# Kernel tuning notes

Hardware: AMD Instinct MI355X
Metric: run time of the kernel (lower is better)

## Reference

```python
import jax, jax.numpy as jnp
import numpy as np

NUM_CODEBOOKS = 8
CODEBOOK_SIZE = 256
DIM = 128
COMMITMENT_WEIGHT = 0.25
B, T = 16, 16384


def setup_inputs() -> dict:
    key = jax.random.key(0)
    k_z, k_cb = jax.random.split(key)
    z = jax.random.normal(k_z, (B, T, DIM), dtype=jnp.float32)
    # nn.init.uniform_(emb.weight, -1/codebook_size, 1/codebook_size)
    bound = 1.0 / CODEBOOK_SIZE
    codebooks = jax.random.uniform(
        k_cb, (NUM_CODEBOOKS, CODEBOOK_SIZE, DIM), dtype=jnp.float32,
        minval=-bound, maxval=bound)
    return {"z": z, "codebooks": codebooks}


def reference(z, codebooks):
    """Residual vector quantization.

    z: [B, T, D] float32
    codebooks: [K, C, D] float32
    Returns (quantized [B,T,D], indices [B,T,K] int32, vq_loss scalar).
    """
    sg = jax.lax.stop_gradient
    residual = z
    vq_loss = jnp.zeros((), dtype=z.dtype)
    quant_sum = jnp.zeros_like(z)
    all_indices = []
    for k in range(NUM_CODEBOOKS):
        cb = codebooks[k]                                   # [C, D]
        # squared euclidean distances: ||r||^2 + ||e||^2 - 2 r.e
        x_sq = jnp.sum(residual * residual, axis=-1, keepdims=True)   # [B,T,1]
        e_sq = jnp.sum(cb * cb, axis=-1)                               # [C]
        cross = jnp.einsum('btd,cd->btc', residual, cb)                # [B,T,C]
        distances = x_sq + e_sq[None, None, :] - 2.0 * cross           # [B,T,C]
        indices = jnp.argmin(distances, axis=-1)                       # [B,T]
        all_indices.append(indices)
        z_q = cb[indices]                                              # [B,T,D] gather
        codebook_loss = jnp.mean((sg(z_q) - residual) ** 2)
        commit_loss = jnp.mean((z_q - sg(residual)) ** 2)
        vq_loss = vq_loss + codebook_loss + COMMITMENT_WEIGHT * commit_loss
        quant_sum = quant_sum + z_q
        residual = residual - sg(z_q)
    indices_stacked = jnp.stack(all_indices, axis=-1)                  # [B,T,K]
    # straight-through estimator
    quantized = z + sg(quant_sum - z)
    return quantized, indices_stacked, vq_loss
```

## Files before the change

### kernel.cpp

```cpp
#include <hip/hip_runtime.h>
#include <hip/hip_bf16.h>
#include <math.h>
#include <float.h>

#define NUM_CB 8
#define CB_SIZE 256
#define DIM 128
#define BT (16 * 16384)
#define Q_ELEMS ((size_t)BT * DIM)
#define I_ELEMS ((size_t)BT * NUM_CB)

#define TC 64
#define TILES_PER_CB (CB_SIZE / TC)
#define TILE_BYTES 32768

#define MARGIN_A 1.5e-4f

typedef short  bf16x8 __attribute__((ext_vector_type(8)));
typedef float  f32x4  __attribute__((ext_vector_type(4)));

__device__ __forceinline__ unsigned short bf16_rne(float f) {
    unsigned int u = __float_as_uint(f);
    u = u + 0x7FFFu + ((u >> 16) & 1u);
    return (unsigned short)(u >> 16);
}
__device__ __forceinline__ float bf16_tof(unsigned short h) {
    return __uint_as_float(((unsigned int)h) << 16);
}
__device__ __forceinline__ unsigned short f2bf(float f) {
    __hip_bfloat16 h = __float2bfloat16(f);
    return *reinterpret_cast<unsigned short*>(&h);
}

__device__ __forceinline__ float np_sum_sq_128(const float* a) {
#pragma clang fp contract(off)
    float r0 = 0.f, r1 = 0.f, r2 = 0.f, r3 = 0.f,
          r4 = 0.f, r5 = 0.f, r6 = 0.f, r7 = 0.f;
#pragma unroll
    for (int i = 0; i < DIM; i += 8) {
        r0 = r0 + a[i + 0] * a[i + 0];
        r1 = r1 + a[i + 1] * a[i + 1];
        r2 = r2 + a[i + 2] * a[i + 2];
        r3 = r3 + a[i + 3] * a[i + 3];
        r4 = r4 + a[i + 4] * a[i + 4];
        r5 = r5 + a[i + 5] * a[i + 5];
        r6 = r6 + a[i + 6] * a[i + 6];
        r7 = r7 + a[i + 7] * a[i + 7];
    }
    return ((r0 + r1) + (r2 + r3)) + ((r4 + r5) + (r6 + r7));
}

__global__ void rvq_esq_kernel(const float* __restrict__ cb,
                               float* __restrict__ esq) {
    int i = blockIdx.x * blockDim.x + threadIdx.x;
    if (i >= NUM_CB * CB_SIZE) return;
    esq[i] = np_sum_sq_128(cb + (size_t)i * DIM);
}

__global__ void rvq_transpose_kernel(const float* __restrict__ cb,
                                     float* __restrict__ cbT) {
    int idx = blockIdx.x * blockDim.x + threadIdx.x;
    if (idx >= NUM_CB * DIM * CB_SIZE) return;
    int c = idx & (CB_SIZE - 1);
    int d = (idx >> 8) & (DIM - 1);
    int k = idx >> 15;
    cbT[idx] = cb[((size_t)(k * CB_SIZE + c)) * DIM + d];
}

__global__ void rvq_split_kernel(const float* __restrict__ cb,
                                 bf16x8* __restrict__ g_img) {
    int idx = blockIdx.x * blockDim.x + threadIdx.x;
    if (idx >= NUM_CB * CB_SIZE * 16) return;
    int slot = idx & 15;
    int cand = (idx >> 4) & (TC - 1);
    int t    = idx >> 10;
    const float* src = cb + ((size_t)t * TC + cand) * DIM + slot * 8;
    float4 a = *reinterpret_cast<const float4*>(src);
    float4 b = *reinterpret_cast<const float4*>(src + 4);
    float e[8] = {a.x, a.y, a.z, a.w, b.x, b.y, b.z, b.w};
    bf16x8 eh, el;
#pragma unroll
    for (int i = 0; i < 8; ++i) {
        unsigned short h = bf16_rne(e[i]);
        float rem = e[i] - bf16_tof(h);
        eh[i] = (short)h;
        el[i] = (short)bf16_rne(rem);
    }
    int ds = slot ^ (cand & 15);
    g_img[(size_t)t * 2048 + cand * 16 + ds]        = eh;
    g_img[(size_t)t * 2048 + 1024 + cand * 16 + ds] = el;
}

__device__ __forceinline__ void stage_tile(const bf16x8* __restrict__ g_img,
                                           bf16x8 (*s_buf)[2048],
                                           int t, int nb, int wid, int lane) {
    const char* gt = (const char*)g_img + (size_t)t * TILE_BYTES
                     + wid * 4096 + lane * 16;
    const char* lb = (const char*)(&s_buf[nb][0]) + wid * 4096;
#pragma unroll
    for (int c = 0; c < 4; ++c) {
        __builtin_amdgcn_global_load_lds(
            (const __attribute__((address_space(1))) unsigned int*)(gt + c * 1024),
            (__attribute__((address_space(3))) unsigned int*)(lb + c * 1024),
            16, 0, 0);
    }
}

__global__ __launch_bounds__(512, 2) void rvq_mfma_kernel(
    const float* __restrict__ z,
    const float* __restrict__ cb,
    const float* __restrict__ cbT,
    const float* __restrict__ esq,
    const bf16x8* __restrict__ g_img,
    float* __restrict__ out_q,
    float* __restrict__ out_idx,
    double* __restrict__ loss_acc) {

    __shared__ bf16x8 s_buf[2][2048];
    __shared__ __align__(16) float s_rbuf[8][DIM];
    __shared__ double s_wsum[8];

    const int tid  = threadIdx.x;
    const int wid  = tid >> 6;
    const int lane = tid & 63;
    const int lrow = lane & 15;
    const int lq   = lane >> 4;
    const int tokw = blockIdx.x * 128 + wid * 16;
    const int tok  = tokw + lrow;

    float r[4][8];
    {
        const float* zp = z + (size_t)tok * DIM + 8 * lq;
#pragma unroll
        for (int s = 0; s < 4; ++s) {
            float4 a = *reinterpret_cast<const float4*>(zp + 32 * s);
            float4 b = *reinterpret_cast<const float4*>(zp + 32 * s + 4);
            r[s][0] = a.x; r[s][1] = a.y; r[s][2] = a.z; r[s][3] = a.w;
            r[s][4] = b.x; r[s][5] = b.y; r[s][6] = b.z; r[s][7] = b.w;
        }
    }

    bf16x8 ah[4], am[4];
#pragma unroll
    for (int s = 0; s < 4; ++s)
#pragma unroll
        for (int i = 0; i < 8; ++i) {
            unsigned short h = f2bf(r[s][i]);
            float rem = r[s][i] - bf16_tof(h);
            ah[s][i] = (short)h;
            am[s][i] = (short)f2bf(rem);
        }

    double lsum = 0.0;

    stage_tile(g_img, s_buf, 0, 0, wid, lane);
    asm volatile("s_waitcnt vmcnt(0)" ::: "memory");
    __syncthreads();

    for (int k = 0; k < NUM_CB; ++k) {
        const float* esqk = esq + k * CB_SIZE;
        const float* cbk  = cb  + (size_t)k * CB_SIZE * DIM;
        const float* cbTk = cbT + (size_t)k * DIM * CB_SIZE + lane;

        float m1 = FLT_MAX, m2 = FLT_MAX;
        int   i1 = 0x7fffffff;

#pragma unroll
        for (int T = 0; T < TILES_PER_CB; ++T) {
            const int t  = k * TILES_PER_CB + T;
            const int nb = T & 1;
            if (k < NUM_CB - 1 || T < TILES_PER_CB - 1)
                stage_tile(g_img, s_buf, t + 1, nb ^ 1, wid, lane);

#pragma unroll
            for (int ctl = 0; ctl < 4; ++ctl) {
                const int ctg  = T * 4 + ctl;
                const int base = (ctl * 16 + lrow) * 16;
                bf16x8 bh[4], bl[4];
#pragma unroll
                for (int s = 0; s < 4; ++s) {
                    int ls = (4 * s + lq) ^ lrow;
                    bh[s] = s_buf[nb][base + ls];
                    bl[s] = s_buf[nb][1024 + base + ls];
                }
                f32x4 acc0 = {0.f, 0.f, 0.f, 0.f};
                f32x4 acc1 = {0.f, 0.f, 0.f, 0.f};
                acc0 = __builtin_amdgcn_mfma_f32_16x16x32_bf16(bh[0], ah[0], acc0, 0, 0, 0);
                acc0 = __builtin_amdgcn_mfma_f32_16x16x32_bf16(bh[1], ah[1], acc0, 0, 0, 0);
                acc1 = __builtin_amdgcn_mfma_f32_16x16x32_bf16(bh[2], ah[2], acc1, 0, 0, 0);
                acc1 = __builtin_amdgcn_mfma_f32_16x16x32_bf16(bh[3], ah[3], acc1, 0, 0, 0);
                acc0 = __builtin_amdgcn_mfma_f32_16x16x32_bf16(bh[0], am[0], acc0, 0, 0, 0);
                acc0 = __builtin_amdgcn_mfma_f32_16x16x32_bf16(bh[1], am[1], acc0, 0, 0, 0);
                acc1 = __builtin_amdgcn_mfma_f32_16x16x32_bf16(bh[2], am[2], acc1, 0, 0, 0);
                acc1 = __builtin_amdgcn_mfma_f32_16x16x32_bf16(bh[3], am[3], acc1, 0, 0, 0);
                acc0 = __builtin_amdgcn_mfma_f32_16x16x32_bf16(bl[0], ah[0], acc0, 0, 0, 0);
                acc0 = __builtin_amdgcn_mfma_f32_16x16x32_bf16(bl[1], ah[1], acc0, 0, 0, 0);
                acc1 = __builtin_amdgcn_mfma_f32_16x16x32_bf16(bl[2], ah[2], acc1, 0, 0, 0);
                acc1 = __builtin_amdgcn_mfma_f32_16x16x32_bf16(bl[3], ah[3], acc1, 0, 0, 0);

                float4 ev = *reinterpret_cast<const float4*>(
                    esqk + ctg * 16 + 4 * lq);
                const float es[4] = {ev.x, ev.y, ev.z, ev.w};
                const int cb0 = ctg * 16 + 4 * lq;
#pragma unroll
                for (int j = 0; j < 4; ++j) {
                    float s = fmaf(-2.0f, acc0[j] + acc1[j], es[j]);
                    m2 = fminf(m2, fmaxf(m1, s));
                    if (s < m1) { m1 = s; i1 = cb0 + j; }
                }
            }

            if (T == TILES_PER_CB - 1) {
#pragma unroll
                for (int d = 16; d < 64; d <<= 1) {
                    float om1 = __shfl_xor(m1, d);
                    float om2 = __shfl_xor(m2, d);
                    int   oi1 = __shfl_xor(i1, d);
                    bool ow = (om1 < m1) || (om1 == m1 && oi1 < i1);
                    float lo = ow ? m1 : om1;
                    m1 = ow ? om1 : m1;
                    i1 = ow ? oi1 : i1;
                    m2 = fminf(fminf(m2, om2), lo);
                }
                int cmin = i1;

                bool amb = !(m2 - m1 > MARGIN_A);
                unsigned long long mask = __ballot(amb && lane < 16);
                while (mask) {
                    int srct = __ffsll(mask) - 1;
                    mask &= mask - 1;
                    if (lrow == srct) {
#pragma unroll
                        for (int s = 0; s < 4; ++s) {
                            float4* dst = reinterpret_cast<float4*>(
                                &s_rbuf[wid][32 * s + 8 * lq]);
                            dst[0] = make_float4(r[s][0], r[s][1], r[s][2], r[s][3]);
                            dst[1] = make_float4(r[s][4], r[s][5], r[s][6], r[s][7]);
                        }
                    }
                    asm volatile("s_waitcnt lgkmcnt(0)" ::: "memory");
                    float xs = 0.f;
                    if (lane == 0) xs = np_sum_sq_128(&s_rbuf[wid][0]);
                    xs = __shfl(xs, 0);

                    const float* rb = &s_rbuf[wid][0];
                    float a0 = 0.f, a1 = 0.f, a2 = 0.f, a3 = 0.f;
#pragma unroll 8
                    for (int d = 0; d < DIM; ++d) {
                        float rv = rb[d];
                        const float* row = cbTk + (size_t)d * CB_SIZE;
                        a0 = fmaf(rv, row[0],   a0);
                        a1 = fmaf(rv, row[64],  a1);
                        a2 = fmaf(rv, row[128], a2);
                        a3 = fmaf(rv, row[192], a3);
                    }
                    float dd0, dd1, dd2, dd3;
                    {
#pragma clang fp contract(off)
                        float S0 = xs + esqk[lane];
                        float S1 = xs + esqk[lane + 64];
                        float S2 = xs + esqk[lane + 128];
                        float S3 = xs + esqk[lane + 192];
                        dd0 = S0 - 2.0f * a0;
                        dd1 = S1 - 2.0f * a1;
                        dd2 = S2 - 2.0f * a2;
                        dd3 = S3 - 2.0f * a3;
                    }
                    float bd = dd0; int bc = lane;
                    if (dd1 < bd) { bd = dd1; bc = lane + 64; }
                    if (dd2 < bd) { bd = dd2; bc = lane + 128; }
                    if (dd3 < bd) { bd = dd3; bc = lane + 192; }
#pragma unroll
                    for (int d = 1; d < 64; d <<= 1) {
                        float od = __shfl_xor(bd, d);
                        int   oc = __shfl_xor(bc, d);
                        if (od < bd || (od == bd && oc < bc)) { bd = od; bc = oc; }
                    }
                    if (lrow == srct) cmin = bc;
                }

                if (lane < 16)
                    out_idx[(size_t)(tokw + lane) * NUM_CB + k] = (float)cmin;

                const float* ep = cbk + (size_t)cmin * DIM + 8 * lq;
                float l0 = 0.f, l1 = 0.f, l2 = 0.f, l3 = 0.f;
#pragma unroll
                for (int s = 0; s < 4; ++s) {
                    float4 ev0 = *reinterpret_cast<const float4*>(ep + 32 * s);
                    float4 ev1 = *reinterpret_cast<const float4*>(ep + 32 * s + 4);
                    float d0 = ev0.x - r[s][0], d1 = ev0.y - r[s][1];
                    float d2 = ev0.z - r[s][2], d3 = ev0.w - r[s][3];
                    float d4 = ev1.x - r[s][4], d5 = ev1.y - r[s][5];
                    float d6 = ev1.z - r[s][6], d7 = ev1.w - r[s][7];
                    l0 = fmaf(d0, d0, l0); l1 = fmaf(d1, d1, l1);
                    l2 = fmaf(d2, d2, l2); l3 = fmaf(d3, d3, l3);
                    l0 = fmaf(d4, d4, l0); l1 = fmaf(d5, d5, l1);
                    l2 = fmaf(d6, d6, l2); l3 = fmaf(d7, d7, l3);
                    r[s][0] -= ev0.x; r[s][1] -= ev0.y; r[s][2] -= ev0.z; r[s][3] -= ev0.w;
                    r[s][4] -= ev1.x; r[s][5] -= ev1.y; r[s][6] -= ev1.z; r[s][7] -= ev1.w;
                }
                lsum += (double)((l0 + l1) + (l2 + l3));

                if (k < NUM_CB - 1) {
#pragma unroll
                    for (int s = 0; s < 4; ++s)
#pragma unroll
                        for (int i = 0; i < 8; ++i) {
                            unsigned short h = f2bf(r[s][i]);
                            float rem = r[s][i] - bf16_tof(h);
                            ah[s][i] = (short)h;
                            am[s][i] = (short)f2bf(rem);
                        }
                }
            }

            asm volatile("s_waitcnt vmcnt(0)" ::: "memory");
            __syncthreads();
        }
    }

    {
        const float* zp = z + (size_t)tok * DIM + 8 * lq;
        float* op = out_q + (size_t)tok * DIM + 8 * lq;
#pragma unroll
        for (int s = 0; s < 4; ++s) {
            float4 a = *reinterpret_cast<const float4*>(zp + 32 * s);
            float4 b = *reinterpret_cast<const float4*>(zp + 32 * s + 4);
            *reinterpret_cast<float4*>(op + 32 * s) =
                make_float4(a.x - r[s][0], a.y - r[s][1],
                            a.z - r[s][2], a.w - r[s][3]);
            *reinterpret_cast<float4*>(op + 32 * s + 4) =
                make_float4(b.x - r[s][4], b.y - r[s][5],
                            b.z - r[s][6], b.w - r[s][7]);
        }
    }

    for (int off = 32; off > 0; off >>= 1)
        lsum += __shfl_down(lsum, off, 64);
    if (lane == 0) s_wsum[wid] = lsum;
    __syncthreads();
    if (tid == 0) {
        double t = 0.0;
#pragma unroll
        for (int w = 0; w < 8; ++w) t += s_wsum[w];
        atomicAdd(loss_acc, t);
    }
}

__global__ void rvq_finalize_kernel(const double* __restrict__ loss_acc,
                                    float* __restrict__ out_loss) {
    out_loss[0] = (float)(1.25 * loss_acc[0] / (double)Q_ELEMS);
}

extern "C" void kernel_launch(void* const* d_in, const int* in_sizes, int n_in,
                              void* d_out, int out_size, void* d_ws, size_t ws_size,
                              hipStream_t stream) {
    const float* z  = (const float*)d_in[0];
    const float* cb = (const float*)d_in[1];

    float* out_q    = (float*)d_out;
    float* out_idx  = out_q + Q_ELEMS;
    float* out_loss = out_idx + I_ELEMS;

    double* loss_acc = (double*)d_ws;
    float*  esq      = (float*)((char*)d_ws + 256);
    bf16x8* g_img    = (bf16x8*)((char*)d_ws + 65536);
    float*  cbT      = (float*)((char*)d_ws + 65536 + 1048576);

    hipMemsetAsync(loss_acc, 0, sizeof(double), stream);
    rvq_esq_kernel<<<(NUM_CB * CB_SIZE + 255) / 256, 256, 0, stream>>>(cb, esq);
    rvq_split_kernel<<<(NUM_CB * CB_SIZE * 16 + 255) / 256, 256, 0, stream>>>(
        cb, g_img);
    rvq_transpose_kernel<<<(NUM_CB * DIM * CB_SIZE + 255) / 256, 256, 0,
                           stream>>>(cb, cbT);
    rvq_mfma_kernel<<<BT / 128, 512, 0, stream>>>(z, cb, cbT, esq, g_img,
                                                  out_q, out_idx, loss_acc);
    rvq_finalize_kernel<<<1, 1, 0, stream>>>(loss_acc, out_loss);
}
```

Measured before the change: 918.2 us.

## Switch distance GEMM to 32x32x16 MFMA with 32 tokens per wave

Measured after the change: 1.018 ms. 10.8% more time.

```diff
diff --git a/kernel.cpp b/kernel.cpp
--- a/kernel.cpp
+++ b/kernel.cpp
@@ -17,7 +17,7 @@
 #define MARGIN_A 1.5e-4f
 
 typedef short  bf16x8 __attribute__((ext_vector_type(8)));
-typedef float  f32x4  __attribute__((ext_vector_type(4)));
+typedef float  f32x16 __attribute__((ext_vector_type(16)));
 
 __device__ __forceinline__ unsigned short bf16_rne(float f) {
     unsigned int u = __float_as_uint(f);
@@ -55,6 +55,18 @@
     int i = blockIdx.x * blockDim.x + threadIdx.x;
     if (i >= NUM_CB * CB_SIZE) return;
     esq[i] = np_sum_sq_128(cb + (size_t)i * DIM);
+}
+
+__global__ void rvq_esqpk_kernel(const float* __restrict__ esq,
+                                 float* __restrict__ esq_pk) {
+    int idx = blockIdx.x * blockDim.x + threadIdx.x;
+    if (idx >= NUM_CB * 8 * 64 * 16) return;
+    int reg  = idx & 15;
+    int lane = (idx >> 4) & 63;
+    int til  = (idx >> 10) & 7;
+    int k    = idx >> 13;
+    esq_pk[idx] = esq[k * CB_SIZE + til * 32 +
+                      (reg & 3) + 8 * (reg >> 2) + 4 * (lane >> 5)];
 }
 
 __global__ void rvq_transpose_kernel(const float* __restrict__ cb,
@@ -95,10 +107,10 @@
                                            bf16x8 (*s_buf)[2048],
                                            int t, int nb, int wid, int lane) {
     const char* gt = (const char*)g_img + (size_t)t * TILE_BYTES
-                     + wid * 4096 + lane * 16;
-    const char* lb = (const char*)(&s_buf[nb][0]) + wid * 4096;
-#pragma unroll
-    for (int c = 0; c < 4; ++c) {
+                     + wid * 8192 + lane * 16;
+    const char* lb = (const char*)(&s_buf[nb][0]) + wid * 8192;
+#pragma unroll
+    for (int c = 0; c < 8; ++c) {
         __builtin_amdgcn_global_load_lds(
             (const __attribute__((address_space(1))) unsigned int*)(gt + c * 1024),
             (__attribute__((address_space(3))) unsigned int*)(lb + c * 1024),
@@ -106,49 +118,49 @@
     }
 }
 
-__global__ __launch_bounds__(512, 2) void rvq_mfma_kernel(
+__global__ __launch_bounds__(256) void rvq_mfma_kernel(
     const float* __restrict__ z,
     const float* __restrict__ cb,
     const float* __restrict__ cbT,
     const float* __restrict__ esq,
+    const float* __restrict__ esq_pk,
     const bf16x8* __restrict__ g_img,
     float* __restrict__ out_q,
     float* __restrict__ out_idx,
     double* __restrict__ loss_acc) {
 
     __shared__ bf16x8 s_buf[2][2048];
-    __shared__ __align__(16) float s_rbuf[8][DIM];
-    __shared__ double s_wsum[8];
+    __shared__ __align__(16) float s_rbuf[4][DIM];
+    __shared__ double s_wsum[4];
 
     const int tid  = threadIdx.x;
     const int wid  = tid >> 6;
     const int lane = tid & 63;
-    const int lrow = lane & 15;
-    const int lq   = lane >> 4;
-    const int tokw = blockIdx.x * 128 + wid * 16;
-    const int tok  = tokw + lrow;
-
-    float r[4][8];
+    const int tk   = lane & 31;
+    const int half = lane >> 5;
+    const int tokw = blockIdx.x * 128 + wid * 32;
+    const int tok  = tokw + tk;
+
+    float r[8][8];
     {
-        const float* zp = z + (size_t)tok * DIM + 8 * lq;
-#pragma unroll
-        for (int s = 0; s < 4; ++s) {
-            float4 a = *reinterpret_cast<const float4*>(zp + 32 * s);
-            float4 b = *reinterpret_cast<const float4*>(zp + 32 * s + 4);
+        const float* zp = z + (size_t)tok * DIM + 8 * half;
+#pragma unroll
+        for (int s = 0; s < 8; ++s) {
+            float4 a = *reinterpret_cast<const float4*>(zp + 16 * s);
+            float4 b = *reinterpret_cast<const float4*>(zp + 16 * s + 4);
             r[s][0] = a.x; r[s][1] = a.y; r[s][2] = a.z; r[s][3] = a.w;
             r[s][4] = b.x; r[s][5] = b.y; r[s][6] = b.z; r[s][7] = b.w;
         }
     }
 
-    bf16x8 ah[4], am[4];
-#pragma unroll
-    for (int s = 0; s < 4; ++s)
+    bf16x8 rh[8], rm[8];
+#pragma unroll
+    for (int s = 0; s < 8; ++s)
 #pragma unroll
         for (int i = 0; i < 8; ++i) {
             unsigned short h = f2bf(r[s][i]);
-            float rem = r[s][i] - bf16_tof(h);
-            ah[s][i] = (short)h;
-            am[s][i] = (short)f2bf(rem);
+            rh[s][i] = (short)h;
+            rm[s][i] = (short)f2bf(r[s][i] - bf16_tof(h));
         }
 
     double lsum = 0.0;
@@ -173,69 +185,68 @@
                 stage_tile(g_img, s_buf, t + 1, nb ^ 1, wid, lane);
 
 #pragma unroll
-            for (int ctl = 0; ctl < 4; ++ctl) {
-                const int ctg  = T * 4 + ctl;
-                const int base = (ctl * 16 + lrow) * 16;
-                bf16x8 bh[4], bl[4];
-#pragma unroll
-                for (int s = 0; s < 4; ++s) {
-                    int ls = (4 * s + lq) ^ lrow;
-                    bh[s] = s_buf[nb][base + ls];
-                    bl[s] = s_buf[nb][1024 + base + ls];
-                }
-                f32x4 acc0 = {0.f, 0.f, 0.f, 0.f};
-                f32x4 acc1 = {0.f, 0.f, 0.f, 0.f};
-                acc0 = __builtin_amdgcn_mfma_f32_16x16x32_bf16(bh[0], ah[0], acc0, 0, 0, 0);
-                acc0 = __builtin_amdgcn_mfma_f32_16x16x32_bf16(bh[1], ah[1], acc0, 0, 0, 0);
-                acc1 = __builtin_amdgcn_mfma_f32_16x16x32_bf16(bh[2], ah[2], acc1, 0, 0, 0);
-                acc1 = __builtin_amdgcn_mfma_f32_16x16x32_bf16(bh[3], ah[3], acc1, 0, 0, 0);
-                acc0 = __builtin_amdgcn_mfma_f32_16x16x32_bf16(bh[0], am[0], acc0, 0, 0, 0);
-                acc0 = __builtin_amdgcn_mfma_f32_16x16x32_bf16(bh[1], am[1], acc0, 0, 0, 0);
-                acc1 = __builtin_amdgcn_mfma_f32_16x16x32_bf16(bh[2], am[2], acc1, 0, 0, 0);
-                acc1 = __builtin_amdgcn_mfma_f32_16x16x32_bf16(bh[3], am[3], acc1, 0, 0, 0);
-                acc0 = __builtin_amdgcn_mfma_f32_16x16x32_bf16(bl[0], ah[0], acc0, 0, 0, 0);
-                acc0 = __builtin_amdgcn_mfma_f32_16x16x32_bf16(bl[1], ah[1], acc0, 0, 0, 0);
-                acc1 = __builtin_amdgcn_mfma_f32_16x16x32_bf16(bl[2], ah[2], acc1, 0, 0, 0);
-                acc1 = __builtin_amdgcn_mfma_f32_16x16x32_bf16(bl[3], ah[3], acc1, 0, 0, 0);
-
-                float4 ev = *reinterpret_cast<const float4*>(
-                    esqk + ctg * 16 + 4 * lq);
-                const float es[4] = {ev.x, ev.y, ev.z, ev.w};
-                const int cb0 = ctg * 16 + 4 * lq;
-#pragma unroll
-                for (int j = 0; j < 4; ++j) {
-                    float s = fmaf(-2.0f, acc0[j] + acc1[j], es[j]);
-                    m2 = fminf(m2, fmaxf(m1, s));
-                    if (s < m1) { m1 = s; i1 = cb0 + j; }
+            for (int u = 0; u < 2; ++u) {
+                const int til = T * 2 + u;
+                const int cand_img = u * 32 + tk;
+                float eq[16];
+                {
+                    const float4* ep4 = reinterpret_cast<const float4*>(
+                        esq_pk + (((size_t)(k * 8 + til) * 64 + lane) * 16));
+#pragma unroll
+                    for (int j = 0; j < 4; ++j) {
+                        float4 v = ep4[j];
+                        eq[4 * j + 0] = v.x; eq[4 * j + 1] = v.y;
+                        eq[4 * j + 2] = v.z; eq[4 * j + 3] = v.w;
+                    }
+                }
+                f32x16 acca = {0.f, 0.f, 0.f, 0.f, 0.f, 0.f, 0.f, 0.f,
+                               0.f, 0.f, 0.f, 0.f, 0.f, 0.f, 0.f, 0.f};
+                f32x16 accb = acca;
+#pragma unroll
+                for (int s = 0; s < 8; ++s) {
+                    const int ls = (2 * s + half) ^ (tk & 15);
+                    bf16x8 eh = s_buf[nb][cand_img * 16 + ls];
+                    bf16x8 el = s_buf[nb][1024 + cand_img * 16 + ls];
+                    acca = __builtin_amdgcn_mfma_f32_32x32x16_bf16(eh, rh[s], acca, 0, 0, 0);
+                    accb = __builtin_amdgcn_mfma_f32_32x32x16_bf16(eh, rm[s], accb, 0, 0, 0);
+                    accb = __builtin_amdgcn_mfma_f32_32x32x16_bf16(el, rh[s], accb, 0, 0, 0);
+                }
+#pragma unroll
+                for (int reg = 0; reg < 16; ++reg) {
+                    const int c = til * 32 + (reg & 3) + 8 * (reg >> 2) + 4 * half;
+                    float sc = fmaf(-2.0f, acca[reg] + accb[reg], eq[reg]);
+                    m2 = __builtin_amdgcn_fmed3f(m1, m2, sc);
+                    if (sc < m1) { i1 = c; }
+                    m1 = fminf(m1, sc);
                 }
             }
 
             if (T == TILES_PER_CB - 1) {
-#pragma unroll
-                for (int d = 16; d < 64; d <<= 1) {
-                    float om1 = __shfl_xor(m1, d);
-                    float om2 = __shfl_xor(m2, d);
-                    int   oi1 = __shfl_xor(i1, d);
-                    bool ow = (om1 < m1) || (om1 == m1 && oi1 < i1);
-                    float lo = ow ? m1 : om1;
-                    m1 = ow ? om1 : m1;
-                    i1 = ow ? oi1 : i1;
-                    m2 = fminf(fminf(m2, om2), lo);
+                {
+                    float o1 = __shfl_xor(m1, 32);
+                    float o2 = __shfl_xor(m2, 32);
+                    int   oi = __shfl_xor(i1, 32);
+                    bool ow = (o1 < m1) || (o1 == m1 && oi < i1);
+                    float lo = ow ? m1 : o1;
+                    m1 = ow ? o1 : m1;
+                    i1 = ow ? oi : i1;
+                    m2 = fminf(fminf(m2, o2), lo);
                 }
                 int cmin = i1;
 
                 bool amb = !(m2 - m1 > MARGIN_A);
-                unsigned long long mask = __ballot(amb && lane < 16);
+                unsigned long long mask = __ballot(amb && lane < 32);
                 while (mask) {
                     int srct = __ffsll(mask) - 1;
                     mask &= mask - 1;
-                    if (lrow == srct) {
-#pragma unroll
-                        for (int s = 0; s < 4; ++s) {
-                            float4* dst = reinterpret_cast<float4*>(
-                                &s_rbuf[wid][32 * s + 8 * lq]);
-                            dst[0] = make_float4(r[s][0], r[s][1], r[s][2], r[s][3]);
-                            dst[1] = make_float4(r[s][4], r[s][5], r[s][6], r[s][7]);
+                    if (tk == srct) {
+#pragma unroll
+                        for (int s = 0; s < 8; ++s) {
+                            float* dst = &s_rbuf[wid][16 * s + 8 * half];
+                            *reinterpret_cast<float4*>(dst) =
+                                make_float4(r[s][0], r[s][1], r[s][2], r[s][3]);
+                            *reinterpret_cast<float4*>(dst + 4) =
+                                make_float4(r[s][4], r[s][5], r[s][6], r[s][7]);
                         }
                     }
                     asm volatile("s_waitcnt lgkmcnt(0)" ::: "memory");
@@ -276,18 +287,18 @@
                         int   oc = __shfl_xor(bc, d);
                         if (od < bd || (od == bd && oc < bc)) { bd = od; bc = oc; }
                     }
-                    if (lrow == srct) cmin = bc;
-                }
-
-                if (lane < 16)
+                    if (tk == srct) cmin = bc;
+                }
+
+                if (lane < 32)
                     out_idx[(size_t)(tokw + lane) * NUM_CB + k] = (float)cmin;
 
-                const float* ep = cbk + (size_t)cmin * DIM + 8 * lq;
+                const float* ep = cbk + (size_t)cmin * DIM + 8 * half;
                 float l0 = 0.f, l1 = 0.f, l2 = 0.f, l3 = 0.f;
 #pragma unroll
-                for (int s = 0; s < 4; ++s) {
-                    float4 ev0 = *reinterpret_cast<const float4*>(ep + 32 * s);
-                    float4 ev1 = *reinterpret_cast<const float4*>(ep + 32 * s + 4);
+                for (int s = 0; s < 8; ++s) {
+                    float4 ev0 = *reinterpret_cast<const float4*>(ep + 16 * s);
+                    float4 ev1 = *reinterpret_cast<const float4*>(ep + 16 * s + 4);
                     float d0 = ev0.x - r[s][0], d1 = ev0.y - r[s][1];
                     float d2 = ev0.z - r[s][2], d3 = ev0.w - r[s][3];
                     float d4 = ev1.x - r[s][4], d5 = ev1.y - r[s][5];
@@ -303,13 +314,12 @@
 
                 if (k < NUM_CB - 1) {
 #pragma unroll
-                    for (int s = 0; s < 4; ++s)
+                    for (int s = 0; s < 8; ++s)
 #pragma unroll
                         for (int i = 0; i < 8; ++i) {
                             unsigned short h = f2bf(r[s][i]);
-                            float rem = r[s][i] - bf16_tof(h);
-                            ah[s][i] = (short)h;
-                            am[s][i] = (short)f2bf(rem);
+                            rh[s][i] = (short)h;
+                            rm[s][i] = (short)f2bf(r[s][i] - bf16_tof(h));
                         }
                 }
             }
@@ -320,16 +330,16 @@
     }
 
     {
-        const float* zp = z + (size_t)tok * DIM + 8 * lq;
-        float* op = out_q + (size_t)tok * DIM + 8 * lq;
-#pragma unroll
-        for (int s = 0; s < 4; ++s) {
-            float4 a = *reinterpret_cast<const float4*>(zp + 32 * s);
-            float4 b = *reinterpret_cast<const float4*>(zp + 32 * s + 4);
-            *reinterpret_cast<float4*>(op + 32 * s) =
+        const float* zp = z + (size_t)tok * DIM + 8 * half;
+        float* op = out_q + (size_t)tok * DIM + 8 * half;
+#pragma unroll
+        for (int s = 0; s < 8; ++s) {
+            float4 a = *reinterpret_cast<const float4*>(zp + 16 * s);
+            float4 b = *reinterpret_cast<const float4*>(zp + 16 * s + 4);
+            *reinterpret_cast<float4*>(op + 16 * s) =
                 make_float4(a.x - r[s][0], a.y - r[s][1],
                             a.z - r[s][2], a.w - r[s][3]);
-            *reinterpret_cast<float4*>(op + 32 * s + 4) =
+            *reinterpret_cast<float4*>(op + 16 * s + 4) =
                 make_float4(b.x - r[s][4], b.y - r[s][5],
                             b.z - r[s][6], b.w - r[s][7]);
         }
@@ -340,10 +350,10 @@
     if (lane == 0) s_wsum[wid] = lsum;
     __syncthreads();
     if (tid == 0) {
-        double t = 0.0;
-#pragma unroll
-        for (int w = 0; w < 8; ++w) t += s_wsum[w];
-        atomicAdd(loss_acc, t);
+        double tt = 0.0;
+#pragma unroll
+        for (int w = 0; w < 4; ++w) tt += s_wsum[w];
+        atomicAdd(loss_acc, tt);
     }
 }
 
@@ -364,16 +374,20 @@
 
     double* loss_acc = (double*)d_ws;
     float*  esq      = (float*)((char*)d_ws + 256);
-    bf16x8* g_img    = (bf16x8*)((char*)d_ws + 65536);
-    float*  cbT      = (float*)((char*)d_ws + 65536 + 1048576);
+    float*  esq_pk   = (float*)((char*)d_ws + 16384);
+    bf16x8* g_img    = (bf16x8*)((char*)d_ws + 294912);
+    float*  cbT      = (float*)((char*)d_ws + 294912 + 1048576);
 
     hipMemsetAsync(loss_acc, 0, sizeof(double), stream);
     rvq_esq_kernel<<<(NUM_CB * CB_SIZE + 255) / 256, 256, 0, stream>>>(cb, esq);
+    rvq_esqpk_kernel<<<(NUM_CB * 8 * 64 * 16 + 255) / 256, 256, 0, stream>>>(
+        esq, esq_pk);
     rvq_split_kernel<<<(NUM_CB * CB_SIZE * 16 + 255) / 256, 256, 0, stream>>>(
         cb, g_img);
     rvq_transpose_kernel<<<(NUM_CB * DIM * CB_SIZE + 255) / 256, 256, 0,
                            stream>>>(cb, cbT);
-    rvq_mfma_kernel<<<BT / 128, 512, 0, stream>>>(z, cb, cbT, esq, g_img,
-                                                  out_q, out_idx, loss_acc);
+    rvq_mfma_kernel<<<BT / 128, 256, 0, stream>>>(z, cb, cbT, esq, esq_pk,
+                                                  g_img, out_q, out_idx,
+                                                  loss_acc);
     rvq_finalize_kernel<<<1, 1, 0, stream>>>(loss_acc, out_loss);
 }
```

## Load codebook MFMA fragments directly from global memory instead of LDS staging

Applied to the files above, without the earlier changes.

Result: no change. 901.8 us (-1.8%).

```diff
diff --git a/kernel.cpp b/kernel.cpp
--- a/kernel.cpp
+++ b/kernel.cpp
@@ -9,10 +9,6 @@
 #define BT (16 * 16384)
 #define Q_ELEMS ((size_t)BT * DIM)
 #define I_ELEMS ((size_t)BT * NUM_CB)
-
-#define TC 64
-#define TILES_PER_CB (CB_SIZE / TC)
-#define TILE_BYTES 32768
 
 #define MARGIN_A 1.5e-4f
 
@@ -67,43 +63,33 @@
     cbT[idx] = cb[((size_t)(k * CB_SIZE + c)) * DIM + d];
 }
 
-__global__ void rvq_split_kernel(const float* __restrict__ cb,
-                                 bf16x8* __restrict__ g_img) {
+__global__ void rvq_split2_kernel(const float* __restrict__ cb,
+                                  bf16x8* __restrict__ g2) {
     int idx = blockIdx.x * blockDim.x + threadIdx.x;
-    if (idx >= NUM_CB * CB_SIZE * 16) return;
-    int slot = idx & 15;
-    int cand = (idx >> 4) & (TC - 1);
-    int t    = idx >> 10;
-    const float* src = cb + ((size_t)t * TC + cand) * DIM + slot * 8;
+    if (idx >= NUM_CB * 16 * 2 * 4 * 64) return;
+    int lane  = idx & 63;
+    int s     = (idx >> 6) & 3;
+    int plane = (idx >> 8) & 1;
+    int ctg   = (idx >> 9) & 15;
+    int k     = idx >> 13;
+    int cand  = ctg * 16 + (lane & 15);
+    int slot  = 4 * s + (lane >> 4);
+    const float* src = cb + ((size_t)(k * CB_SIZE + cand)) * DIM + slot * 8;
     float4 a = *reinterpret_cast<const float4*>(src);
     float4 b = *reinterpret_cast<const float4*>(src + 4);
     float e[8] = {a.x, a.y, a.z, a.w, b.x, b.y, b.z, b.w};
-    bf16x8 eh, el;
+    bf16x8 v;
 #pragma unroll
     for (int i = 0; i < 8; ++i) {
         unsigned short h = bf16_rne(e[i]);
-        float rem = e[i] - bf16_tof(h);
-        eh[i] = (short)h;
-        el[i] = (short)bf16_rne(rem);
-    }
-    int ds = slot ^ (cand & 15);
-    g_img[(size_t)t * 2048 + cand * 16 + ds]        = eh;
-    g_img[(size_t)t * 2048 + 1024 + cand * 16 + ds] = el;
-}
-
-__device__ __forceinline__ void stage_tile(const bf16x8* __restrict__ g_img,
-                                           bf16x8 (*s_buf)[2048],
-                                           int t, int nb, int wid, int lane) {
-    const char* gt = (const char*)g_img + (size_t)t * TILE_BYTES
-                     + wid * 4096 + lane * 16;
-    const char* lb = (const char*)(&s_buf[nb][0]) + wid * 4096;
-#pragma unroll
-    for (int c = 0; c < 4; ++c) {
-        __builtin_amdgcn_global_load_lds(
-            (const __attribute__((address_space(1))) unsigned int*)(gt + c * 1024),
-            (__attribute__((address_space(3))) unsigned int*)(lb + c * 1024),
-            16, 0, 0);
-    }
+        if (plane == 0) {
+            v[i] = (short)h;
+        } else {
+            float rem = e[i] - bf16_tof(h);
+            v[i] = (short)bf16_rne(rem);
+        }
+    }
+    g2[idx] = v;
 }
 
 __global__ __launch_bounds__(512, 2) void rvq_mfma_kernel(
@@ -111,12 +97,11 @@
     const float* __restrict__ cb,
     const float* __restrict__ cbT,
     const float* __restrict__ esq,
-    const bf16x8* __restrict__ g_img,
+    const bf16x8* __restrict__ g2,
     float* __restrict__ out_q,
     float* __restrict__ out_idx,
     double* __restrict__ loss_acc) {
 
-    __shared__ bf16x8 s_buf[2][2048];
     __shared__ __align__(16) float s_rbuf[8][DIM];
     __shared__ double s_wsum[8];
 
@@ -153,10 +138,6 @@
 
     double lsum = 0.0;
 
-    stage_tile(g_img, s_buf, 0, 0, wid, lane);
-    asm volatile("s_waitcnt vmcnt(0)" ::: "memory");
-    __syncthreads();
-
     for (int k = 0; k < NUM_CB; ++k) {
         const float* esqk = esq + k * CB_SIZE;
         const float* cbk  = cb  + (size_t)k * CB_SIZE * DIM;
@@ -165,157 +146,142 @@
         float m1 = FLT_MAX, m2 = FLT_MAX;
         int   i1 = 0x7fffffff;
 
-#pragma unroll
-        for (int T = 0; T < TILES_PER_CB; ++T) {
-            const int t  = k * TILES_PER_CB + T;
-            const int nb = T & 1;
-            if (k < NUM_CB - 1 || T < TILES_PER_CB - 1)
-                stage_tile(g_img, s_buf, t + 1, nb ^ 1, wid, lane);
-
-#pragma unroll
-            for (int ctl = 0; ctl < 4; ++ctl) {
-                const int ctg  = T * 4 + ctl;
-                const int base = (ctl * 16 + lrow) * 16;
-                bf16x8 bh[4], bl[4];
+#pragma unroll 4
+        for (int ctg = 0; ctg < 16; ++ctg) {
+            const bf16x8* gp = g2 + ((size_t)(k * 16 + ctg) * 8 * 64) + lane;
+            bf16x8 bh[4], bl[4];
+#pragma unroll
+            for (int s = 0; s < 4; ++s) {
+                bh[s] = gp[s * 64];
+                bl[s] = gp[(4 + s) * 64];
+            }
+            f32x4 acc0 = {0.f, 0.f, 0.f, 0.f};
+            f32x4 acc1 = {0.f, 0.f, 0.f, 0.f};
+            acc0 = __builtin_amdgcn_mfma_f32_16x16x32_bf16(bh[0], ah[0], acc0, 0, 0, 0);
+            acc0 = __builtin_amdgcn_mfma_f32_16x16x32_bf16(bh[1], ah[1], acc0, 0, 0, 0);
+            acc1 = __builtin_amdgcn_mfma_f32_16x16x32_bf16(bh[2], ah[2], acc1, 0, 0, 0);
+            acc1 = __builtin_amdgcn_mfma_f32_16x16x32_bf16(bh[3], ah[3], acc1, 0, 0, 0);
+            acc0 = __builtin_amdgcn_mfma_f32_16x16x32_bf16(bh[0], am[0], acc0, 0, 0, 0);
+            acc0 = __builtin_amdgcn_mfma_f32_16x16x32_bf16(bh[1], am[1], acc0, 0, 0, 0);
+            acc1 = __builtin_amdgcn_mfma_f32_16x16x32_bf16(bh[2], am[2], acc1, 0, 0, 0);
+            acc1 = __builtin_amdgcn_mfma_f32_16x16x32_bf16(bh[3], am[3], acc1, 0, 0, 0);
+            acc0 = __builtin_amdgcn_mfma_f32_16x16x32_bf16(bl[0], ah[0], acc0, 0, 0, 0);
+            acc0 = __builtin_amdgcn_mfma_f32_16x16x32_bf16(bl[1], ah[1], acc0, 0, 0, 0);
+            acc1 = __builtin_amdgcn_mfma_f32_16x16x32_bf16(bl[2], ah[2], acc1, 0, 0, 0);
+            acc1 = __builtin_amdgcn_mfma_f32_16x16x32_bf16(bl[3], ah[3], acc1, 0, 0, 0);
+
+            float4 ev = *reinterpret_cast<const float4*>(
+                esqk + ctg * 16 + 4 * lq);
+            const float es[4] = {ev.x, ev.y, ev.z, ev.w};
+            const int cb0 = ctg * 16 + 4 * lq;
+#pragma unroll
+            for (int j = 0; j < 4; ++j) {
+                float s = fmaf(-2.0f, acc0[j] + acc1[j], es[j]);
+                m2 = fminf(m2, fmaxf(m1, s));
+                if (s < m1) { m1 = s; i1 = cb0 + j; }
+            }
+        }
+
+#pragma unroll
+        for (int d = 16; d < 64; d <<= 1) {
+            float om1 = __shfl_xor(m1, d);
+            float om2 = __shfl_xor(m2, d);
+            int   oi1 = __shfl_xor(i1, d);
+            bool ow = (om1 < m1) || (om1 == m1 && oi1 < i1);
+            float lo = ow ? m1 : om1;
+            m1 = ow ? om1 : m1;
+            i1 = ow ? oi1 : i1;
+            m2 = fminf(fminf(m2, om2), lo);
+        }
+        int cmin = i1;
+
+        bool amb = !(m2 - m1 > MARGIN_A);
+        unsigned long long mask = __ballot(amb && lane < 16);
+        while (mask) {
+            int srct = __ffsll(mask) - 1;
+            mask &= mask - 1;
+            if (lrow == srct) {
 #pragma unroll
                 for (int s = 0; s < 4; ++s) {
-                    int ls = (4 * s + lq) ^ lrow;
-                    bh[s] = s_buf[nb][base + ls];
-                    bl[s] = s_buf[nb][1024 + base + ls];
+                    float4* dst = reinterpret_cast<float4*>(
+                        &s_rbuf[wid][32 * s + 8 * lq]);
+                    dst[0] = make_float4(r[s][0], r[s][1], r[s][2], r[s][3]);
+                    dst[1] = make_float4(r[s][4], r[s][5], r[s][6], r[s][7]);
                 }
-                f32x4 acc0 = {0.f, 0.f, 0.f, 0.f};
-                f32x4 acc1 = {0.f, 0.f, 0.f, 0.f};
-                acc0 = __builtin_amdgcn_mfma_f32_16x16x32_bf16(bh[0], ah[0], acc0, 0, 0, 0);
-                acc0 = __builtin_amdgcn_mfma_f32_16x16x32_bf16(bh[1], ah[1], acc0, 0, 0, 0);
-                acc1 = __builtin_amdgcn_mfma_f32_16x16x32_bf16(bh[2], ah[2], acc1, 0, 0, 0);
-                acc1 = __builtin_amdgcn_mfma_f32_16x16x32_bf16(bh[3], ah[3], acc1, 0, 0, 0);
-                acc0 = __builtin_amdgcn_mfma_f32_16x16x32_bf16(bh[0], am[0], acc0, 0, 0, 0);
-                acc0 = __builtin_amdgcn_mfma_f32_16x16x32_bf16(bh[1], am[1], acc0, 0, 0, 0);
-                acc1 = __builtin_amdgcn_mfma_f32_16x16x32_bf16(bh[2], am[2], acc1, 0, 0, 0);
-                acc1 = __builtin_amdgcn_mfma_f32_16x16x32_bf16(bh[3], am[3], acc1, 0, 0, 0);
-                acc0 = __builtin_amdgcn_mfma_f32_16x16x32_bf16(bl[0], ah[0], acc0, 0, 0, 0);
-                acc0 = __builtin_amdgcn_mfma_f32_16x16x32_bf16(bl[1], ah[1], acc0, 0, 0, 0);
-                acc1 = __builtin_amdgcn_mfma_f32_16x16x32_bf16(bl[2], ah[2], acc1, 0, 0, 0);
-                acc1 = __builtin_amdgcn_mfma_f32_16x16x32_bf16(bl[3], ah[3], acc1, 0, 0, 0);
-
-                float4 ev = *reinterpret_cast<const float4*>(
-                    esqk + ctg * 16 + 4 * lq);
-                const float es[4] = {ev.x, ev.y, ev.z, ev.w};
-                const int cb0 = ctg * 16 + 4 * lq;
-#pragma unroll
-                for (int j = 0; j < 4; ++j) {
-                    float s = fmaf(-2.0f, acc0[j] + acc1[j], es[j]);
-                    m2 = fminf(m2, fmaxf(m1, s));
-                    if (s < m1) { m1 = s; i1 = cb0 + j; }
+            }
+            asm volatile("s_waitcnt lgkmcnt(0)" ::: "memory");
+            float xs = 0.f;
+            if (lane == 0) xs = np_sum_sq_128(&s_rbuf[wid][0]);
+            xs = __shfl(xs, 0);
+
+            const float* rb = &s_rbuf[wid][0];
+            float a0 = 0.f, a1 = 0.f, a2 = 0.f, a3 = 0.f;
+#pragma unroll 8
+            for (int d = 0; d < DIM; ++d) {
+                float rv = rb[d];
+                const float* row = cbTk + (size_t)d * CB_SIZE;
+                a0 = fmaf(rv, row[0],   a0);
+                a1 = fmaf(rv, row[64],  a1);
+                a2 = fmaf(rv, row[128], a2);
+                a3 = fmaf(rv, row[192], a3);
+            }
+            float dd0, dd1, dd2, dd3;
+            {
+#pragma clang fp contract(off)
+                float S0 = xs + esqk[lane];
+                float S1 = xs + esqk[lane + 64];
+                float S2 = xs + esqk[lane + 128];
+                float S3 = xs + esqk[lane + 192];
+                dd0 = S0 - 2.0f * a0;
+                dd1 = S1 - 2.0f * a1;
+                dd2 = S2 - 2.0f * a2;
+                dd3 = S3 - 2.0f * a3;
+            }
+            float bd = dd0; int bc = lane;
+            if (dd1 < bd) { bd = dd1; bc = lane + 64; }
+            if (dd2 < bd) { bd = dd2; bc = lane + 128; }
+            if (dd3 < bd) { bd = dd3; bc = lane + 192; }
+#pragma unroll
+            for (int d = 1; d < 64; d <<= 1) {
+                float od = __shfl_xor(bd, d);
+                int   oc = __shfl_xor(bc, d);
+                if (od < bd || (od == bd && oc < bc)) { bd = od; bc = oc; }
+            }
+            if (lrow == srct) cmin = bc;
+        }
+
+        if (lane < 16)
+            out_idx[(size_t)(tokw + lane) * NUM_CB + k] = (float)cmin;
+
+        const float* ep = cbk + (size_t)cmin * DIM + 8 * lq;
+        float l0 = 0.f, l1 = 0.f, l2 = 0.f, l3 = 0.f;
+#pragma unroll
+        for (int s = 0; s < 4; ++s) {
+            float4 ev0 = *reinterpret_cast<const float4*>(ep + 32 * s);
+            float4 ev1 = *reinterpret_cast<const float4*>(ep + 32 * s + 4);
+            float d0 = ev0.x - r[s][0], d1 = ev0.y - r[s][1];
+            float d2 = ev0.z - r[s][2], d3 = ev0.w - r[s][3];
+            float d4 = ev1.x - r[s][4], d5 = ev1.y - r[s][5];
+            float d6 = ev1.z - r[s][6], d7 = ev1.w - r[s][7];
+            l0 = fmaf(d0, d0, l0); l1 = fmaf(d1, d1, l1);
+            l2 = fmaf(d2, d2, l2); l3 = fmaf(d3, d3, l3);
+            l0 = fmaf(d4, d4, l0); l1 = fmaf(d5, d5, l1);
+            l2 = fmaf(d6, d6, l2); l3 = fmaf(d7, d7, l3);
+            r[s][0] -= ev0.x; r[s][1] -= ev0.y; r[s][2] -= ev0.z; r[s][3] -= ev0.w;
+            r[s][4] -= ev1.x; r[s][5] -= ev1.y; r[s][6] -= ev1.z; r[s][7] -= ev1.w;
+        }
+        lsum += (double)((l0 + l1) + (l2 + l3));
+
+        if (k < NUM_CB - 1) {
+#pragma unroll
+            for (int s = 0; s < 4; ++s)
+#pragma unroll
+                for (int i = 0; i < 8; ++i) {
+                    unsigned short h = f2bf(r[s][i]);
+                    float rem = r[s][i] - bf16_tof(h);
+                    ah[s][i] = (short)h;
+                    am[s][i] = (short)f2bf(rem);
                 }
-            }
-
-            if (T == TILES_PER_CB - 1) {
-#pragma unroll
-                for (int d = 16; d < 64; d <<= 1) {
-                    float om1 = __shfl_xor(m1, d);
-                    float om2 = __shfl_xor(m2, d);
-                    int   oi1 = __shfl_xor(i1, d);
-                    bool ow = (om1 < m1) || (om1 == m1 && oi1 < i1);
-                    float lo = ow ? m1 : om1;
-                    m1 = ow ? om1 : m1;
-                    i1 = ow ? oi1 : i1;
-                    m2 = fminf(fminf(m2, om2), lo);
-                }
-                int cmin = i1;
-
-                bool amb = !(m2 - m1 > MARGIN_A);
-                unsigned long long mask = __ballot(amb && lane < 16);
-                while (mask) {
-                    int srct = __ffsll(mask) - 1;
-                    mask &= mask - 1;
-                    if (lrow == srct) {
-#pragma unroll
-                        for (int s = 0; s < 4; ++s) {
-                            float4* dst = reinterpret_cast<float4*>(
-                                &s_rbuf[wid][32 * s + 8 * lq]);
-                            dst[0] = make_float4(r[s][0], r[s][1], r[s][2], r[s][3]);
-                            dst[1] = make_float4(r[s][4], r[s][5], r[s][6], r[s][7]);
-                        }
-                    }
-                    asm volatile("s_waitcnt lgkmcnt(0)" ::: "memory");
-                    float xs = 0.f;
-                    if (lane == 0) xs = np_sum_sq_128(&s_rbuf[wid][0]);
-                    xs = __shfl(xs, 0);
-
-                    const float* rb = &s_rbuf[wid][0];
-                    float a0 = 0.f, a1 = 0.f, a2 = 0.f, a3 = 0.f;
-#pragma unroll 8
-                    for (int d = 0; d < DIM; ++d) {
-                        float rv = rb[d];
-                        const float* row = cbTk + (size_t)d * CB_SIZE;
-                        a0 = fmaf(rv, row[0],   a0);
-                        a1 = fmaf(rv, row[64],  a1);
-                        a2 = fmaf(rv, row[128], a2);
-                        a3 = fmaf(rv, row[192], a3);
-                    }
-                    float dd0, dd1, dd2, dd3;
-                    {
-#pragma clang fp contract(off)
-                        float S0 = xs + esqk[lane];
-                        float S1 = xs + esqk[lane + 64];
-                        float S2 = xs + esqk[lane + 128];
-                        float S3 = xs + esqk[lane + 192];
-                        dd0 = S0 - 2.0f * a0;
-                        dd1 = S1 - 2.0f * a1;
-                        dd2 = S2 - 2.0f * a2;
-                        dd3 = S3 - 2.0f * a3;
-                    }
-                    float bd = dd0; int bc = lane;
-                    if (dd1 < bd) { bd = dd1; bc = lane + 64; }
-                    if (dd2 < bd) { bd = dd2; bc = lane + 128; }
-                    if (dd3 < bd) { bd = dd3; bc = lane + 192; }
-#pragma unroll
-                    for (int d = 1; d < 64; d <<= 1) {
-                        float od = __shfl_xor(bd, d);
-                        int   oc = __shfl_xor(bc, d);
-                        if (od < bd || (od == bd && oc < bc)) { bd = od; bc = oc; }
-                    }
-                    if (lrow == srct) cmin = bc;
-                }
-
-                if (lane < 16)
-                    out_idx[(size_t)(tokw + lane) * NUM_CB + k] = (float)cmin;
-
-                const float* ep = cbk + (size_t)cmin * DIM + 8 * lq;
-                float l0 = 0.f, l1 = 0.f, l2 = 0.f, l3 = 0.f;
-#pragma unroll
-                for (int s = 0; s < 4; ++s) {
-                    float4 ev0 = *reinterpret_cast<const float4*>(ep + 32 * s);
-                    float4 ev1 = *reinterpret_cast<const float4*>(ep + 32 * s + 4);
-                    float d0 = ev0.x - r[s][0], d1 = ev0.y - r[s][1];
-                    float d2 = ev0.z - r[s][2], d3 = ev0.w - r[s][3];
-                    float d4 = ev1.x - r[s][4], d5 = ev1.y - r[s][5];
-                    float d6 = ev1.z - r[s][6], d7 = ev1.w - r[s][7];
-                    l0 = fmaf(d0, d0, l0); l1 = fmaf(d1, d1, l1);
-                    l2 = fmaf(d2, d2, l2); l3 = fmaf(d3, d3, l3);
-                    l0 = fmaf(d4, d4, l0); l1 = fmaf(d5, d5, l1);
-                    l2 = fmaf(d6, d6, l2); l3 = fmaf(d7, d7, l3);
-                    r[s][0] -= ev0.x; r[s][1] -= ev0.y; r[s][2] -= ev0.z; r[s][3] -= ev0.w;
-                    r[s][4] -= ev1.x; r[s][5] -= ev1.y; r[s][6] -= ev1.z; r[s][7] -= ev1.w;
-                }
-                lsum += (double)((l0 + l1) + (l2 + l3));
-
-                if (k < NUM_CB - 1) {
-#pragma unroll
-                    for (int s = 0; s < 4; ++s)
-#pragma unroll
-                        for (int i = 0; i < 8; ++i) {
-                            unsigned short h = f2bf(r[s][i]);
-                            float rem = r[s][i] - bf16_tof(h);
-                            ah[s][i] = (short)h;
-                            am[s][i] = (short)f2bf(rem);
-                        }
-                }
-            }
-
-            asm volatile("s_waitcnt vmcnt(0)" ::: "memory");
-            __syncthreads();
         }
     }
 
@@ -364,16 +330,16 @@
 
     double* loss_acc = (double*)d_ws;
     float*  esq      = (float*)((char*)d_ws + 256);
-    bf16x8* g_img    = (bf16x8*)((char*)d_ws + 65536);
+    bf16x8* g2       = (bf16x8*)((char*)d_ws + 65536);
     float*  cbT      = (float*)((char*)d_ws + 65536 + 1048576);
 
     hipMemsetAsync(loss_acc, 0, sizeof(double), stream);
     rvq_esq_kernel<<<(NUM_CB * CB_SIZE + 255) / 256, 256, 0, stream>>>(cb, esq);
-    rvq_split_kernel<<<(NUM_CB * CB_SIZE * 16 + 255) / 256, 256, 0, stream>>>(
-        cb, g_img);
+    rvq_split2_kernel<<<(NUM_CB * 16 * 2 * 4 * 64 + 255) / 256, 256, 0,
+                        stream>>>(cb, g2);
     rvq_transpose_kernel<<<(NUM_CB * DIM * CB_SIZE + 255) / 256, 256, 0,
                            stream>>>(cb, cbT);
-    rvq_mfma_kernel<<<BT / 128, 512, 0, stream>>>(z, cb, cbT, esq, g_img,
+    rvq_mfma_kernel<<<BT / 128, 512, 0, stream>>>(z, cb, cbT, esq, g2,
                                                   out_q, out_idx, loss_acc);
     rvq_finalize_kernel<<<1, 1, 0, stream>>>(loss_acc, out_loss);
 }
```
